# Kernel tuning notes

Hardware: AMD Instinct MI355X
Metric: run time of the kernel (lower is better)

Reference implementation:

```python
import jax, jax.numpy as jnp
import numpy as np

DIM = 192
SCALE = DIM ** (-0.5)


def setup_inputs() -> dict:
    key = jax.random.key(0)
    qkv = jax.random.normal(key, (8, 4096, 3 * DIM), dtype=jnp.float32)
    return {"qkv": qkv}


def reference(qkv):
    # qkv: [B, T, 3C] -> q, k, v each [B, T, C]
    q, k, v = jnp.split(qkv, 3, axis=2)
    # scale_in=True: scale q and k before distance computation
    q = q * SCALE
    k = k * SCALE
    # L2-distance attention logits: -||q_t - k_s||_2, computed via the
    # expansion ||q||^2 + ||k||^2 - 2 q.k (same as torch.cdist for large inputs)
    q2 = jnp.sum(q * q, axis=-1)          # [B, T]
    k2 = jnp.sum(k * k, axis=-1)          # [B, S]
    d2 = q2[:, :, None] + k2[:, None, :] - 2.0 * jnp.einsum('btc,bsc->bts', q, k)
    d2 = jnp.maximum(d2, 0.0)
    # safe sqrt (zero distance on the diagonal since q and k come from same tokens)
    dist = jnp.where(d2 > 0, jnp.sqrt(jnp.where(d2 > 0, d2, 1.0)), 0.0)
    attn_logits = -dist                    # [B, T, S]
    attn = jax.nn.softmax(attn_logits, axis=-1)
    return jnp.einsum('bts,bsc->btc', attn, v)  # [B, T, C]
```

## Files before the change

### kernel.cpp

```cpp
#include <hip/hip_runtime.h>
#include <hip/hip_bf16.h>


#define BB 8
#define TT 4096
#define CD 192

typedef __attribute__((ext_vector_type(8))) _Float16 half8;
typedef __attribute__((ext_vector_type(4))) _Float16 half4;
typedef __attribute__((ext_vector_type(8))) short short8;
typedef __attribute__((ext_vector_type(4))) float float4v;
typedef __attribute__((ext_vector_type(2))) unsigned int uint2v;

constexpr float A2C = (float)(2.0813689810056077 / 192.0);
constexpr float M2A2C = -2.0f * A2C;

static __device__ __forceinline__ unsigned short f2h(float f) {
  return __builtin_bit_cast(unsigned short, (_Float16)f);
}
static __device__ __forceinline__ float h2f(unsigned short u) {
  return (float)__builtin_bit_cast(_Float16, u);
}

__global__ __launch_bounds__(256) void prep(
    const float* __restrict__ qkv, short8* __restrict__ qsw,
    short8* __restrict__ ksw, short8* __restrict__ vsw,
    float* __restrict__ q2A, float* __restrict__ k2A) {
  __shared__ unsigned short tile[32 * 584];
  const int t = threadIdx.x;
  const int b = blockIdx.x >> 7;
  const int sc = blockIdx.x & 127;
  const float* src = qkv + ((size_t)(b * TT + sc * 32)) * (3 * CD);
#pragma unroll
  for (int j = 0; j < 18; ++j) {
    int f = j * 256 + t;
    int row = f / 144, c4 = (f % 144) * 4;
    float4v x = *(const float4v*)(src + (size_t)row * 576 + c4);
    unsigned r0 = (unsigned)f2h(x[0]) | ((unsigned)f2h(x[1]) << 16);
    unsigned r1 = (unsigned)f2h(x[2]) | ((unsigned)f2h(x[3]) << 16);
    *(uint2v*)&tile[row * 584 + c4] = (uint2v){r0, r1};
  }
  __syncthreads();

  const int lane = t & 63, w = t >> 6;
  const int L = lane & 15, q = lane >> 4;
  const int which = w >> 1;
  const int s16o = w & 1;
  const int row = s16o * 16 + L;
  short8* dst = which ? ksw : qsw;
  const size_t ubase = ((size_t)(b * 256 + sc * 2 + s16o)) * 6;
  float ss = 0.f;
#pragma unroll
  for (int ch = 0; ch < 6; ++ch) {
    short8 fr = *(const short8*)&tile[row * 584 + which * CD + ch * 32 + q * 8];
#pragma unroll
    for (int j = 0; j < 8; ++j) {
      float f = h2f((unsigned short)fr[j]);
      ss += f * f;
    }
    dst[(ubase + ch) * 64 + lane] = fr;
  }
  ss += __shfl_xor(ss, 16);
  ss += __shfl_xor(ss, 32);
  if (lane < 16)
    (which ? k2A : q2A)[b * TT + sc * 32 + s16o * 16 + lane] = ss * A2C;

#pragma unroll
  for (int i = 0; i < 3; ++i) {
    int ct = w * 3 + i;
    short8 fr;
#pragma unroll
    for (int j = 0; j < 4; ++j) {
      fr[j]     = (short)tile[(4 * q + j) * 584 + 2 * CD + ct * 16 + L];
      fr[j + 4] = (short)tile[(16 + 4 * q + j) * 584 + 2 * CD + ct * 16 + L];
    }
    vsw[((size_t)(b * 12 + ct) * 128 + sc) * 64 + lane] = fr;
  }
}

__global__ __launch_bounds__(256, 2) void attn3(
    const short8* __restrict__ qsw, const short8* __restrict__ ksw,
    const short8* __restrict__ vsw, const float* __restrict__ q2A,
    const float* __restrict__ k2A, float* __restrict__ out) {
  __shared__ __align__(16) unsigned char s_lds[36864];

  const int tid = threadIdx.x;
  const int w = tid >> 6;
  const int lane = tid & 63;
  const int L = lane & 15;
  const int q = lane >> 4;
  const int b = blockIdx.x & 7;
  const int h = (blockIdx.x >> 3) & 1;
  const int qt = blockIdx.x >> 4;
  const int q0 = qt * 128 + w * 32;
  const size_t bT = (size_t)b * TT;

  auto stage = [&](int it, int buf) {
#pragma unroll
    for (int j = 0; j < 5; ++j) {
      int u = w + 4 * j;
      if (u < 12) {
        int so = u / 6, ch = u % 6;
        const char* ga = (const char*)ksw +
            (((size_t)(b * 256 + it * 2 + so) * 6 + ch) * 64 + lane) * 16;
        char* la = (char*)s_lds + buf * 12288 + u * 1024;
        __builtin_amdgcn_global_load_lds(
            (const __attribute__((address_space(1))) void*)ga,
            (__attribute__((address_space(3))) void*)la, 16, 0, 0);
      } else if (u < 18) {
        int j2 = u - 12;
        const char* ga = (const char*)vsw +
            (((size_t)(b * 12 + h * 6 + j2) * 128 + it) * 64 + lane) * 16;
        char* la = (char*)s_lds + 24576 + buf * 6144 + j2 * 1024;
        __builtin_amdgcn_global_load_lds(
            (const __attribute__((address_space(1))) void*)ga,
            (__attribute__((address_space(3))) void*)la, 16, 0, 0);
      }
    }
  };

  half8 qf[2][6];
#pragma unroll
  for (int mt = 0; mt < 2; ++mt)
#pragma unroll
    for (int ch = 0; ch < 6; ++ch)
      qf[mt][ch] = __builtin_bit_cast(
          half8, qsw[((size_t)(b * 256 + (q0 >> 4) + mt) * 6 + ch) * 64 + lane]);

  float q2l[2];
  q2l[0] = q2A[bT + q0 + L];
  q2l[1] = q2A[bT + q0 + 16 + L];

  float4v oacc[2][6];
#pragma unroll
  for (int mt = 0; mt < 2; ++mt)
#pragma unroll
    for (int ct = 0; ct < 6; ++ct) oacc[mt][ct] = (float4v){0.f, 0.f, 0.f, 0.f};
  float lsum[2] = {0.f, 0.f};

  stage(0, 0);
  __syncthreads();

#pragma unroll 1
  for (int it = 0; it < 128; ++it) {
    const int cur = it & 1;
    if (it + 1 < 128) stage(it + 1, cur ^ 1);
    const int s0 = it * 32;

    float4v k2l[2];
    k2l[0] = *(const float4v*)(k2A + bT + s0 + 4 * q);
    k2l[1] = *(const float4v*)(k2A + bT + s0 + 16 + 4 * q);

    float4v sacc[2][2];
#pragma unroll
    for (int mt = 0; mt < 2; ++mt)
#pragma unroll
      for (int n = 0; n < 2; ++n) sacc[mt][n] = (float4v){0.f, 0.f, 0.f, 0.f};
#pragma unroll
    for (int ch = 0; ch < 6; ++ch) {
      half8 kf0 = *(const half8*)(s_lds + cur * 12288 + ch * 1024 + lane * 16);
      half8 kf1 = *(const half8*)(s_lds + cur * 12288 + (6 + ch) * 1024 + lane * 16);
      sacc[0][0] = __builtin_amdgcn_mfma_f32_16x16x32_f16(kf0, qf[0][ch], sacc[0][0], 0, 0, 0);
      sacc[0][1] = __builtin_amdgcn_mfma_f32_16x16x32_f16(kf1, qf[0][ch], sacc[0][1], 0, 0, 0);
      sacc[1][0] = __builtin_amdgcn_mfma_f32_16x16x32_f16(kf0, qf[1][ch], sacc[1][0], 0, 0, 0);
      sacc[1][1] = __builtin_amdgcn_mfma_f32_16x16x32_f16(kf1, qf[1][ch], sacc[1][1], 0, 0, 0);
    }

    half4 paf[2][2];
#pragma unroll
    for (int mt = 0; mt < 2; ++mt)
#pragma unroll
      for (int n = 0; n < 2; ++n) {
        float4v pv;
#pragma unroll
        for (int r = 0; r < 4; ++r) {
          float tt = fmaf(sacc[mt][n][r], M2A2C, q2l[mt] + k2l[n][r]);
          float p = __builtin_amdgcn_exp2f(-__builtin_amdgcn_sqrtf(fmaxf(tt, 0.f)));
          lsum[mt] += p;
          pv[r] = p;
        }
        paf[mt][n] = (half4){(_Float16)pv[0], (_Float16)pv[1],
                             (_Float16)pv[2], (_Float16)pv[3]};
      }

#pragma unroll
    for (int ct = 0; ct < 6; ++ct) {
      half8 vv = *(const half8*)(s_lds + 24576 + cur * 6144 + ct * 1024 + lane * 16);
      half4 vlo = __builtin_shufflevector(vv, vv, 0, 1, 2, 3);
      half4 vhi = __builtin_shufflevector(vv, vv, 4, 5, 6, 7);
      oacc[0][ct] = __builtin_amdgcn_mfma_f32_16x16x16f16(paf[0][0], vlo, oacc[0][ct], 0, 0, 0);
      oacc[0][ct] = __builtin_amdgcn_mfma_f32_16x16x16f16(paf[0][1], vhi, oacc[0][ct], 0, 0, 0);
      oacc[1][ct] = __builtin_amdgcn_mfma_f32_16x16x16f16(paf[1][0], vlo, oacc[1][ct], 0, 0, 0);
      oacc[1][ct] = __builtin_amdgcn_mfma_f32_16x16x16f16(paf[1][1], vhi, oacc[1][ct], 0, 0, 0);
    }

    __syncthreads();
  }

#pragma unroll
  for (int mt = 0; mt < 2; ++mt) {
    float ls = lsum[mt];
    ls += __shfl_xor(ls, 16);
    ls += __shfl_xor(ls, 32);
#pragma unroll
    for (int r = 0; r < 4; ++r) {
      float linv = 1.f / __shfl(ls, 4 * q + r);
#pragma unroll
      for (int ct = 0; ct < 6; ++ct)
        out[(bT + q0 + mt * 16 + 4 * q + r) * CD + (h * 6 + ct) * 16 + L] =
            oacc[mt][ct][r] * linv;
    }
  }
}

extern "C" void kernel_launch(void* const* d_in, const int* in_sizes, int n_in,
                              void* d_out, int out_size, void* d_ws, size_t ws_size,
                              hipStream_t stream) {
  (void)in_sizes; (void)n_in; (void)out_size; (void)ws_size;
  const float* qkv = (const float*)d_in[0];
  float* out = (float*)d_out;

  short8* qsw = (short8*)d_ws;
  short8* ksw = qsw + (size_t)BB * 256 * 6 * 64;
  short8* vsw = ksw + (size_t)BB * 256 * 6 * 64;
  float* q2A = (float*)(vsw + (size_t)BB * 12 * 128 * 64);
  float* k2A = q2A + (size_t)BB * TT;

  prep<<<BB * 128, 256, 0, stream>>>(qkv, qsw, ksw, vsw, q2A, k2A);
  attn3<<<BB * 64, 256, 0, stream>>>(qsw, ksw, vsw, q2A, k2A, out);
}
```

Baseline: 299.7 us.

## Split attention over key halves instead of channel halves, add combine kernel

```diff
diff --git a/kernel.cpp b/kernel.cpp
--- a/kernel.cpp
+++ b/kernel.cpp
@@ -78,11 +78,12 @@
   }
 }
 
-__global__ __launch_bounds__(256, 2) void attn3(
+__global__ __launch_bounds__(256, 2) void attn4(
     const short8* __restrict__ qsw, const short8* __restrict__ ksw,
     const short8* __restrict__ vsw, const float* __restrict__ q2A,
-    const float* __restrict__ k2A, float* __restrict__ out) {
-  __shared__ __align__(16) unsigned char s_lds[36864];
+    const float* __restrict__ k2A, float* __restrict__ out,
+    float* __restrict__ opart1, float* __restrict__ lpart) {
+  __shared__ __align__(16) unsigned char s_lds[49152];
 
   const int tid = threadIdx.x;
   const int w = tid >> 6;
@@ -90,28 +91,28 @@
   const int L = lane & 15;
   const int q = lane >> 4;
   const int b = blockIdx.x & 7;
-  const int h = (blockIdx.x >> 3) & 1;
+  const int sk = (blockIdx.x >> 3) & 1;
   const int qt = blockIdx.x >> 4;
   const int q0 = qt * 128 + w * 32;
   const size_t bT = (size_t)b * TT;
 
-  auto stage = [&](int it, int buf) {
-#pragma unroll
-    for (int j = 0; j < 5; ++j) {
-      int u = w + 4 * j;
+  auto stage = [&](int itg, int buf) {
+#pragma unroll
+    for (int j = 0; j < 6; ++j) {
+      int u = w * 6 + j;
       if (u < 12) {
         int so = u / 6, ch = u % 6;
         const char* ga = (const char*)ksw +
-            (((size_t)(b * 256 + it * 2 + so) * 6 + ch) * 64 + lane) * 16;
+            (((size_t)(b * 256 + itg * 2 + so) * 6 + ch) * 64 + lane) * 16;
         char* la = (char*)s_lds + buf * 12288 + u * 1024;
         __builtin_amdgcn_global_load_lds(
             (const __attribute__((address_space(1))) void*)ga,
             (__attribute__((address_space(3))) void*)la, 16, 0, 0);
-      } else if (u < 18) {
-        int j2 = u - 12;
+      } else {
+        int ct = u - 12;
         const char* ga = (const char*)vsw +
-            (((size_t)(b * 12 + h * 6 + j2) * 128 + it) * 64 + lane) * 16;
-        char* la = (char*)s_lds + 24576 + buf * 6144 + j2 * 1024;
+            (((size_t)(b * 12 + ct) * 128 + itg) * 64 + lane) * 16;
+        char* la = (char*)s_lds + 24576 + buf * 12288 + ct * 1024;
         __builtin_amdgcn_global_load_lds(
             (const __attribute__((address_space(1))) void*)ga,
             (__attribute__((address_space(3))) void*)la, 16, 0, 0);
@@ -131,21 +132,21 @@
   q2l[0] = q2A[bT + q0 + L];
   q2l[1] = q2A[bT + q0 + 16 + L];
 
-  float4v oacc[2][6];
+  float4v oacc[2][12];
 #pragma unroll
   for (int mt = 0; mt < 2; ++mt)
 #pragma unroll
-    for (int ct = 0; ct < 6; ++ct) oacc[mt][ct] = (float4v){0.f, 0.f, 0.f, 0.f};
+    for (int ct = 0; ct < 12; ++ct) oacc[mt][ct] = (float4v){0.f, 0.f, 0.f, 0.f};
   float lsum[2] = {0.f, 0.f};
 
-  stage(0, 0);
+  stage(sk * 64, 0);
   __syncthreads();
 
 #pragma unroll 1
-  for (int it = 0; it < 128; ++it) {
+  for (int it = 0; it < 64; ++it) {
     const int cur = it & 1;
-    if (it + 1 < 128) stage(it + 1, cur ^ 1);
-    const int s0 = it * 32;
+    if (it + 1 < 64) stage(sk * 64 + it + 1, cur ^ 1);
+    const int s0 = sk * 2048 + it * 32;
 
     float4v k2l[2];
     k2l[0] = *(const float4v*)(k2A + bT + s0 + 4 * q);
@@ -175,7 +176,7 @@
 #pragma unroll
         for (int r = 0; r < 4; ++r) {
           float tt = fmaf(sacc[mt][n][r], M2A2C, q2l[mt] + k2l[n][r]);
-          float p = __builtin_amdgcn_exp2f(-__builtin_amdgcn_sqrtf(fmaxf(tt, 0.f)));
+          float p = __builtin_amdgcn_exp2f(-__builtin_amdgcn_sqrtf(__builtin_fabsf(tt)));
           lsum[mt] += p;
           pv[r] = p;
         }
@@ -184,8 +185,8 @@
       }
 
 #pragma unroll
-    for (int ct = 0; ct < 6; ++ct) {
-      half8 vv = *(const half8*)(s_lds + 24576 + cur * 6144 + ct * 1024 + lane * 16);
+    for (int ct = 0; ct < 12; ++ct) {
+      half8 vv = *(const half8*)(s_lds + 24576 + cur * 12288 + ct * 1024 + lane * 16);
       half4 vlo = __builtin_shufflevector(vv, vv, 0, 1, 2, 3);
       half4 vhi = __builtin_shufflevector(vv, vv, 4, 5, 6, 7);
       oacc[0][ct] = __builtin_amdgcn_mfma_f32_16x16x16f16(paf[0][0], vlo, oacc[0][ct], 0, 0, 0);
@@ -197,20 +198,33 @@
     __syncthreads();
   }
 
+  float* odst = sk ? opart1 : out;
 #pragma unroll
   for (int mt = 0; mt < 2; ++mt) {
     float ls = lsum[mt];
     ls += __shfl_xor(ls, 16);
     ls += __shfl_xor(ls, 32);
-#pragma unroll
-    for (int r = 0; r < 4; ++r) {
-      float linv = 1.f / __shfl(ls, 4 * q + r);
-#pragma unroll
-      for (int ct = 0; ct < 6; ++ct)
-        out[(bT + q0 + mt * 16 + 4 * q + r) * CD + (h * 6 + ct) * 16 + L] =
-            oacc[mt][ct][r] * linv;
-    }
-  }
+    if (lane < 16)
+      lpart[(size_t)sk * (BB * TT) + bT + q0 + mt * 16 + L] = ls;
+#pragma unroll
+    for (int r = 0; r < 4; ++r)
+#pragma unroll
+      for (int ct = 0; ct < 12; ++ct)
+        odst[(bT + q0 + mt * 16 + 4 * q + r) * CD + ct * 16 + L] =
+            oacc[mt][ct][r];
+  }
+}
+
+__global__ __launch_bounds__(256) void combine(
+    float* __restrict__ out, const float* __restrict__ opart1,
+    const float* __restrict__ lpart) {
+  int idx = blockIdx.x * 256 + threadIdx.x;
+  int row = idx / 48;
+  float linv = 1.f / (lpart[row] + lpart[BB * TT + row]);
+  float4v a = *(const float4v*)(out + (size_t)idx * 4);
+  float4v c = *(const float4v*)(opart1 + (size_t)idx * 4);
+  float4v r = (a + c) * linv;
+  *(float4v*)(out + (size_t)idx * 4) = r;
 }
 
 extern "C" void kernel_launch(void* const* d_in, const int* in_sizes, int n_in,
@@ -225,7 +239,10 @@
   short8* vsw = ksw + (size_t)BB * 256 * 6 * 64;
   float* q2A = (float*)(vsw + (size_t)BB * 12 * 128 * 64);
   float* k2A = q2A + (size_t)BB * TT;
+  float* opart1 = k2A + (size_t)BB * TT;
+  float* lpart = opart1 + (size_t)BB * TT * CD;
 
   prep<<<BB * 128, 256, 0, stream>>>(qkv, qsw, ksw, vsw, q2A, k2A);
-  attn3<<<BB * 64, 256, 0, stream>>>(qsw, ksw, vsw, q2A, k2A, out);
-}
+  attn4<<<BB * 64, 256, 0, stream>>>(qsw, ksw, vsw, q2A, k2A, out, opart1, lpart);
+  combine<<<BB * TT * (CD / 4) / 256, 256, 0, stream>>>(out, opart1, lpart);
+}
```

Result: faster. 246.9 us (-17.6%).
